# Optimization experiments

Measured on AMD Instinct MI355X. Metric: run time of the kernel, lower is better.

## Reference

```python
import jax, jax.numpy as jnp
import numpy as np

NEG_SLOPE = 0.2  # DGL GATConv default negative_slope


def gat_conv(x, W, attn_l, attn_r, bias, src, dst, n_nodes):
    """DGL-style GATConv. x:[N,F_in], W:[F_in,H*D], attn_l/attn_r/bias:[H,D].
    Returns [N,H,D]."""
    H, D = attn_l.shape
    feat = (x @ W).reshape(n_nodes, H, D)            # projected features
    el = jnp.sum(feat * attn_l, axis=-1)              # [N,H]
    er = jnp.sum(feat * attn_r, axis=-1)              # [N,H]
    e = jax.nn.leaky_relu(el[src] + er[dst], NEG_SLOPE)  # [E,H] per-edge score
    # edge softmax over incoming edges of each dst node (numerically stable)
    m = jax.ops.segment_max(e, dst, num_segments=n_nodes)   # [N,H]
    a = jnp.exp(e - m[dst])
    denom = jax.ops.segment_sum(a, dst, num_segments=n_nodes)
    alpha = a / denom[dst]                            # [E,H]
    msg = feat[src] * alpha[..., None]                # [E,H,D]
    out = jax.ops.segment_sum(msg, dst, num_segments=n_nodes)  # [N,H,D]
    return out + bias


def setup_inputs() -> dict:
    key = jax.random.key(0)
    ks = jax.random.split(key, 12)
    N, E = 50000, 800000
    F_in, D1, H1, F_out = 128, 32, 4, 64
    h = jax.random.normal(ks[0], (N, F_in), dtype=jnp.float32)
    src = jax.random.randint(ks[1], (E,), 0, N, dtype=jnp.int32)
    dst = jax.random.randint(ks[2], (E,), 0, N, dtype=jnp.int32)
    s1 = 1.0 / np.sqrt(F_in)
    s2 = 1.0 / np.sqrt(H1 * D1)
    W1 = jax.random.normal(ks[3], (F_in, H1 * D1), dtype=jnp.float32) * s1
    al1 = jax.random.normal(ks[4], (H1, D1), dtype=jnp.float32) * s1
    ar1 = jax.random.normal(ks[5], (H1, D1), dtype=jnp.float32) * s1
    b1 = jnp.zeros((H1, D1), dtype=jnp.float32)
    W2 = jax.random.normal(ks[6], (H1 * D1, 1 * F_out), dtype=jnp.float32) * s2
    al2 = jax.random.normal(ks[7], (1, F_out), dtype=jnp.float32) * s2
    ar2 = jax.random.normal(ks[8], (1, F_out), dtype=jnp.float32) * s2
    b2 = jnp.zeros((1, F_out), dtype=jnp.float32)
    return {"h": h, "src": src, "dst": dst,
            "W1": W1, "al1": al1, "ar1": ar1, "b1": b1,
            "W2": W2, "al2": al2, "ar2": ar2, "b2": b2}


def reference(h, src, dst, W1, al1, ar1, b1, W2, al2, ar2, b2):
    N = h.shape[0]
    x = gat_conv(h, W1, al1, ar1, b1, src, dst, N)   # [N,H,D]
    x = jax.nn.relu(x.reshape(N, -1))                # flatten heads + ReLU
    # dropout(p=0.2) is identity in eval mode
    x = gat_conv(x, W2, al2, ar2, b2, src, dst, N)   # [N,1,F_out]
    return x.squeeze(1)
```

## Files before the change

kernel.cpp:

```cpp
#include <hip/hip_runtime.h>

#define NEG_SLOPE 0.2f
#define CH 4096
#define DCAP 2048

__device__ inline unsigned short f2bf(float f) {
    unsigned u = __float_as_uint(f);
    unsigned r = (u + 0x7FFFu + ((u >> 16) & 1u)) >> 16;
    return (unsigned short)r;
}
__device__ inline float bf2f(unsigned short s) {
    return __uint_as_float(((unsigned)s) << 16);
}
__device__ inline void wave_lds_fence() {
    asm volatile("s_waitcnt lgkmcnt(0)" ::: "memory");
}

__global__ __launch_bounds__(256) void bucketA_kernel(const int* __restrict__ dst,
                                                      int* __restrict__ bucket_cnt,
                                                      int E, int NB) {
    __shared__ int lh[1024];
    const int tid = threadIdx.x;
    for (int i = tid; i < 1024; i += 256) lh[i] = 0;
    __syncthreads();
    const int base = blockIdx.x * CH;
    const int cnt = min(CH, E - base);
    for (int i = tid; i < cnt; i += 256) atomicAdd(&lh[dst[base + i] >> 6], 1);
    __syncthreads();
    for (int b = tid; b < NB; b += 256)
        if (lh[b]) atomicAdd(&bucket_cnt[b], lh[b]);
}

__global__ __launch_bounds__(1024) void bucketB_kernel(const int* __restrict__ bucket_cnt,
                                                       int* __restrict__ bucket_base,
                                                       int* __restrict__ bucket_cursor,
                                                       int* __restrict__ row_start,
                                                       int N, int NB, int E) {
    __shared__ int sh[1024];
    const int tid = threadIdx.x;
    int v = (tid < NB) ? bucket_cnt[tid] : 0;
    sh[tid] = v;
    __syncthreads();
    for (int off = 1; off < 1024; off <<= 1) {
        int t = (tid >= off) ? sh[tid - off] : 0;
        __syncthreads();
        sh[tid] += t;
        __syncthreads();
    }
    int ex = sh[tid] - v;
    if (tid < NB) {
        bucket_base[tid] = ex;
        bucket_cursor[tid] = ex;
    }
    if (tid == NB - 1) bucket_base[NB] = ex + v;
    if (tid == 0) row_start[N] = E;
}

__global__ __launch_bounds__(256) void csrC_gemm1_kernel(
    const int* __restrict__ src, const int* __restrict__ dst,
    int* __restrict__ bucket_cursor, unsigned* __restrict__ tmp, int E, int NB,
    int nchunks, const float* __restrict__ h, const float* __restrict__ W1,
    const float* __restrict__ al1, const float* __restrict__ ar1,
    unsigned short* __restrict__ feat1b, float* __restrict__ el1,
    float* __restrict__ er1, int N) {
    __shared__ __align__(16) int smem[8448];
    const int tid = threadIdx.x;
    if ((int)blockIdx.x < nchunks) {
        int* lh = smem;
        int* lex = smem + 1024;
        int* lcur = smem + 2048;
        int* gbase_sh = smem + 3072;
        int* psum = smem + 4096;
        unsigned* sortedv = (unsigned*)(smem + 4352);
        const int base_e = blockIdx.x * CH;
        const int cnt_e = min(CH, E - base_e);
        for (int i = tid; i < 1024; i += 256) lh[i] = 0;
        __syncthreads();
        for (int i = tid; i < cnt_e; i += 256) atomicAdd(&lh[dst[base_e + i] >> 6], 1);
        __syncthreads();
        int s0 = lh[tid * 4], s1 = lh[tid * 4 + 1], s2 = lh[tid * 4 + 2], s3 = lh[tid * 4 + 3];
        int tot = s0 + s1 + s2 + s3;
        psum[tid] = tot;
        __syncthreads();
        for (int off = 1; off < 256; off <<= 1) {
            int t = (tid >= off) ? psum[tid - off] : 0;
            __syncthreads();
            psum[tid] += t;
            __syncthreads();
        }
        int ebase = psum[tid] - tot;
        lex[tid * 4] = ebase;
        lex[tid * 4 + 1] = ebase + s0;
        lex[tid * 4 + 2] = ebase + s0 + s1;
        lex[tid * 4 + 3] = ebase + s0 + s1 + s2;
        __syncthreads();
        for (int b = tid; b < NB; b += 256) {
            int c = lh[b];
            gbase_sh[b] = c ? atomicAdd(&bucket_cursor[b], c) : 0;
            lcur[b] = 0;
        }
        __syncthreads();
        for (int i = tid; i < cnt_e; i += 256) {
            int e = base_e + i;
            int d = dst[e];
            unsigned b = (unsigned)d >> 6;
            int r = atomicAdd(&lcur[b], 1);
            sortedv[lex[b] + r] =
                (b << 22) | ((unsigned)(d & 63) << 16) | (unsigned)(src[e] & 0xFFFF);
        }
        __syncthreads();
        for (int i = tid; i < cnt_e; i += 256) {
            unsigned v = sortedv[i];
            int b = v >> 22;
            tmp[gbase_sh[b] + (i - lex[b])] = v;
        }
    } else {
        float* xs = (float*)smem;
        const int row0 = ((int)blockIdx.x - nchunks) * 64;
        {
            const float4* s4 = (const float4*)h;
            float4* d4 = (float4*)xs;
            int base4 = row0 * 32;
            int tot4 = N * 32;
            for (int i = tid; i < 2048; i += 256)
                if (base4 + i < tot4) d4[i] = s4[base4 + i];
        }
        __syncthreads();
        const int lane = tid & 31;
        const int c0 = lane * 4;
        const int r0 = (tid >> 5) * 8;
        float acc[8][4] = {};
#pragma unroll 4
        for (int k = 0; k < 128; ++k) {
            float4 w = *(const float4*)(W1 + k * 128 + c0);
#pragma unroll
            for (int r = 0; r < 8; ++r) {
                float x = xs[(r0 + r) * 128 + k];
                acc[r][0] = fmaf(x, w.x, acc[r][0]);
                acc[r][1] = fmaf(x, w.y, acc[r][1]);
                acc[r][2] = fmaf(x, w.z, acc[r][2]);
                acc[r][3] = fmaf(x, w.w, acc[r][3]);
            }
        }
        float4 alv = *(const float4*)(al1 + c0);
        float4 arv = *(const float4*)(ar1 + c0);
#pragma unroll
        for (int r = 0; r < 8; ++r) {
            int row = row0 + r0 + r;
            if (row < N) {
                ushort4 fb;
                fb.x = f2bf(acc[r][0]);
                fb.y = f2bf(acc[r][1]);
                fb.z = f2bf(acc[r][2]);
                fb.w = f2bf(acc[r][3]);
                *(ushort4*)(feat1b + (size_t)row * 128 + c0) = fb;
                float pl = acc[r][0] * alv.x + acc[r][1] * alv.y + acc[r][2] * alv.z +
                           acc[r][3] * alv.w;
                float pr = acc[r][0] * arv.x + acc[r][1] * arv.y + acc[r][2] * arv.z +
                           acc[r][3] * arv.w;
#pragma unroll
                for (int off = 4; off >= 1; off >>= 1) {
                    pl += __shfl_xor(pl, off, 32);
                    pr += __shfl_xor(pr, off, 32);
                }
                if ((lane & 7) == 0) {
                    el1[row * 4 + (lane >> 3)] = pl;
                    er1[row * 4 + (lane >> 3)] = pr;
                }
            }
        }
    }
}

__global__ __launch_bounds__(256) void bucketD_kernel(const unsigned* __restrict__ tmp,
                                                      const int* __restrict__ bucket_base,
                                                      int* __restrict__ srcs,
                                                      int* __restrict__ row_start,
                                                      int N, int NB) {
    __shared__ unsigned sval[DCAP];
    __shared__ int ssrc[DCAP];
    __shared__ int dh[64], dex[64], dcur[64];
    const int b = blockIdx.x;
    const int tid = threadIdx.x;
    const int gb = bucket_base[b], ge = bucket_base[b + 1];
    const int cnt = ge - gb;
    if (tid < 64) dh[tid] = 0;
    __syncthreads();
    if (cnt <= DCAP) {
        for (int i = tid; i < cnt; i += 256) {
            unsigned v = tmp[gb + i];
            sval[i] = v;
            atomicAdd(&dh[(v >> 16) & 63], 1);
        }
        __syncthreads();
        if (tid < 64) {
            int v = dh[tid], inc = v;
            for (int off = 1; off < 64; off <<= 1) {
                int t = __shfl_up(inc, off, 64);
                if (tid >= off) inc += t;
            }
            dex[tid] = inc - v;
            dcur[tid] = 0;
            int dglob = b * 64 + tid;
            if (dglob < N) row_start[dglob] = gb + inc - v;
        }
        __syncthreads();
        for (int i = tid; i < cnt; i += 256) {
            unsigned val = sval[i];
            int dl = (val >> 16) & 63;
            int r = atomicAdd(&dcur[dl], 1);
            ssrc[dex[dl] + r] = (int)(val & 0xFFFFu);
        }
        __syncthreads();
        for (int i = tid; i < cnt; i += 256) srcs[gb + i] = ssrc[i];
    } else {
        for (int i = tid; i < cnt; i += 256) atomicAdd(&dh[(tmp[gb + i] >> 16) & 63], 1);
        __syncthreads();
        if (tid < 64) {
            int v = dh[tid], inc = v;
            for (int off = 1; off < 64; off <<= 1) {
                int t = __shfl_up(inc, off, 64);
                if (tid >= off) inc += t;
            }
            dex[tid] = inc - v;
            dcur[tid] = 0;
            int dglob = b * 64 + tid;
            if (dglob < N) row_start[dglob] = gb + inc - v;
        }
        __syncthreads();
        for (int i = tid; i < cnt; i += 256) {
            unsigned val = tmp[gb + i];
            int dl = (val >> 16) & 63;
            int r = atomicAdd(&dcur[dl], 1);
            srcs[gb + dex[dl] + r] = (int)(val & 0xFFFFu);
        }
    }
}

__global__ __launch_bounds__(256) void gemm2_fused(const unsigned short* __restrict__ out1b,
                                                   const float* __restrict__ W2,
                                                   const float* __restrict__ al2,
                                                   const float* __restrict__ ar2,
                                                   unsigned short* __restrict__ feat2b,
                                                   float* __restrict__ el2,
                                                   float* __restrict__ er2, int N) {
    __shared__ float xs[128 * 128];
    const int tid = threadIdx.x;
    const int row0 = blockIdx.x * 128;
    {
        const uint4* s8 = (const uint4*)out1b;
        int base8 = row0 * 16;
        int tot8 = N * 16;
        for (int i = tid; i < 2048; i += 256)
            if (base8 + i < tot8) {
                uint4 v = s8[base8 + i];
                float* o = xs + i * 8;
                o[0] = bf2f((unsigned short)(v.x & 0xFFFF));
                o[1] = bf2f((unsigned short)(v.x >> 16));
                o[2] = bf2f((unsigned short)(v.y & 0xFFFF));
                o[3] = bf2f((unsigned short)(v.y >> 16));
                o[4] = bf2f((unsigned short)(v.z & 0xFFFF));
                o[5] = bf2f((unsigned short)(v.z >> 16));
                o[6] = bf2f((unsigned short)(v.w & 0xFFFF));
                o[7] = bf2f((unsigned short)(v.w >> 16));
            }
    }
    __syncthreads();
    const int lane = tid & 15;
    const int c0 = lane * 4;
    const int r0 = (tid >> 4) * 8;
    float acc[8][4] = {};
#pragma unroll 4
    for (int k = 0; k < 128; ++k) {
        float4 w = *(const float4*)(W2 + k * 64 + c0);
#pragma unroll
        for (int r = 0; r < 8; ++r) {
            float x = xs[(r0 + r) * 128 + k];
            acc[r][0] = fmaf(x, w.x, acc[r][0]);
            acc[r][1] = fmaf(x, w.y, acc[r][1]);
            acc[r][2] = fmaf(x, w.z, acc[r][2]);
            acc[r][3] = fmaf(x, w.w, acc[r][3]);
        }
    }
    float4 alv = *(const float4*)(al2 + c0);
    float4 arv = *(const float4*)(ar2 + c0);
#pragma unroll
    for (int r = 0; r < 8; ++r) {
        int row = row0 + r0 + r;
        if (row < N) {
            ushort4 fb;
            fb.x = f2bf(acc[r][0]);
            fb.y = f2bf(acc[r][1]);
            fb.z = f2bf(acc[r][2]);
            fb.w = f2bf(acc[r][3]);
            *(ushort4*)(feat2b + (size_t)row * 64 + c0) = fb;
            float pl = acc[r][0] * alv.x + acc[r][1] * alv.y + acc[r][2] * alv.z +
                       acc[r][3] * alv.w;
            float pr = acc[r][0] * arv.x + acc[r][1] * arv.y + acc[r][2] * arv.z +
                       acc[r][3] * arv.w;
#pragma unroll
            for (int off = 8; off >= 1; off >>= 1) {
                pl += __shfl_xor(pl, off, 16);
                pr += __shfl_xor(pr, off, 16);
            }
            if (lane == 0) {
                el2[row] = pl;
                er2[row] = pr;
            }
        }
    }
}

__global__ __launch_bounds__(256) void gather1_kernel(const int* __restrict__ row_start,
                                                      const int* __restrict__ srcs,
                                                      const float* __restrict__ el1,
                                                      const float* __restrict__ er1,
                                                      const unsigned short* __restrict__ feat1b,
                                                      const float* __restrict__ b1,
                                                      unsigned short* __restrict__ out1b,
                                                      int N) {
    __shared__ int s_sh[4][64];
    __shared__ float a_sh[4][256];
    const int tid = threadIdx.x;
    const int w = tid >> 6;
    const int lane = tid & 63;
    const int d = blockIdx.x * 4 + w;
    if (d >= N) return;
    const int beg = row_start[d], end = row_start[d + 1];
    const int half = lane >> 5;
    const int l32 = lane & 31;
    const int c0 = l32 * 4;
    const int h = l32 >> 3;
    float4 er4 = *(const float4*)(er1 + (size_t)d * 4);
    float acc0 = 0.f, acc1 = 0.f, acc2 = 0.f, acc3 = 0.f;
    float bcc0 = 0.f, bcc1 = 0.f, bcc2 = 0.f, bcc3 = 0.f;
    float den = 0.f;
    for (int k0 = beg; k0 < end; k0 += 64) {
        const int M = min(64, end - k0);
        if (lane < M) {
            int s = srcs[k0 + lane];
            s_sh[w][lane] = s;
            float4 el4 = *(const float4*)(el1 + (size_t)s * 4);
            float v0 = el4.x + er4.x;
            float v1 = el4.y + er4.y;
            float v2 = el4.z + er4.z;
            float v3 = el4.w + er4.w;
            v0 = v0 > 0.f ? v0 : NEG_SLOPE * v0;
            v1 = v1 > 0.f ? v1 : NEG_SLOPE * v1;
            v2 = v2 > 0.f ? v2 : NEG_SLOPE * v2;
            v3 = v3 > 0.f ? v3 : NEG_SLOPE * v3;
            a_sh[w][lane * 4 + 0] = __expf(v0);
            a_sh[w][lane * 4 + 1] = __expf(v1);
            a_sh[w][lane * 4 + 2] = __expf(v2);
            a_sh[w][lane * 4 + 3] = __expf(v3);
        }
        wave_lds_fence();
        int e = half;
        for (; e + 2 < M; e += 4) {
            int s0 = s_sh[w][e], s1 = s_sh[w][e + 2];
            float a0 = a_sh[w][e * 4 + h];
            float a1 = a_sh[w][(e + 2) * 4 + h];
            ushort4 f0 = *(const ushort4*)(feat1b + (size_t)s0 * 128 + c0);
            ushort4 f1 = *(const ushort4*)(feat1b + (size_t)s1 * 128 + c0);
            den += a0 + a1;
            acc0 = fmaf(bf2f(f0.x), a0, acc0);
            acc1 = fmaf(bf2f(f0.y), a0, acc1);
            acc2 = fmaf(bf2f(f0.z), a0, acc2);
            acc3 = fmaf(bf2f(f0.w), a0, acc3);
            bcc0 = fmaf(bf2f(f1.x), a1, bcc0);
            bcc1 = fmaf(bf2f(f1.y), a1, bcc1);
            bcc2 = fmaf(bf2f(f1.z), a1, bcc2);
            bcc3 = fmaf(bf2f(f1.w), a1, bcc3);
        }
        if (e < M) {
            int s0 = s_sh[w][e];
            float a0 = a_sh[w][e * 4 + h];
            ushort4 f0 = *(const ushort4*)(feat1b + (size_t)s0 * 128 + c0);
            den += a0;
            acc0 = fmaf(bf2f(f0.x), a0, acc0);
            acc1 = fmaf(bf2f(f0.y), a0, acc1);
            acc2 = fmaf(bf2f(f0.z), a0, acc2);
            acc3 = fmaf(bf2f(f0.w), a0, acc3);
        }
        wave_lds_fence();
    }
    acc0 += bcc0;
    acc1 += bcc1;
    acc2 += bcc2;
    acc3 += bcc3;
    acc0 += __shfl_xor(acc0, 32, 64);
    acc1 += __shfl_xor(acc1, 32, 64);
    acc2 += __shfl_xor(acc2, 32, 64);
    acc3 += __shfl_xor(acc3, 32, 64);
    den += __shfl_xor(den, 32, 64);
    if (half == 0) {
        float inv = (end > beg) ? 1.f / den : 0.f;
        float4 bv = *(const float4*)(b1 + c0);
        float r0v = fmaxf(acc0 * inv + bv.x, 0.f);
        float r1v = fmaxf(acc1 * inv + bv.y, 0.f);
        float r2v = fmaxf(acc2 * inv + bv.z, 0.f);
        float r3v = fmaxf(acc3 * inv + bv.w, 0.f);
        ushort4 o;
        o.x = f2bf(r0v);
        o.y = f2bf(r1v);
        o.z = f2bf(r2v);
        o.w = f2bf(r3v);
        *(ushort4*)(out1b + (size_t)d * 128 + c0) = o;
    }
}

__global__ __launch_bounds__(256) void gather2_kernel(const int* __restrict__ row_start,
                                                      const int* __restrict__ srcs,
                                                      const float* __restrict__ el2,
                                                      const float* __restrict__ er2,
                                                      const unsigned short* __restrict__ feat2b,
                                                      const float* __restrict__ b2,
                                                      float* __restrict__ out2, int N) {
    __shared__ int s_sh[4][64];
    __shared__ float a_sh[4][64];
    const int tid = threadIdx.x;
    const int w = tid >> 6;
    const int lane = tid & 63;
    const int d = blockIdx.x * 4 + w;
    if (d >= N) return;
    const int beg = row_start[d], end = row_start[d + 1];
    const int half = lane >> 5;
    const int l32 = lane & 31;
    const int c0 = l32 * 2;
    const float er_d = er2[d];
    float acc0 = 0.f, acc1 = 0.f, bcc0 = 0.f, bcc1 = 0.f, den = 0.f;
    for (int k0 = beg; k0 < end; k0 += 64) {
        const int M = min(64, end - k0);
        if (lane < M) {
            int s = srcs[k0 + lane];
            s_sh[w][lane] = s;
            float v = el2[s] + er_d;
            v = v > 0.f ? v : NEG_SLOPE * v;
            a_sh[w][lane] = __expf(v);
        }
        wave_lds_fence();
        int e = half;
        for (; e + 2 < M; e += 4) {
            int s0 = s_sh[w][e], s1 = s_sh[w][e + 2];
            float a0 = a_sh[w][e], a1 = a_sh[w][e + 2];
            ushort2 f0 = *(const ushort2*)(feat2b + (size_t)s0 * 64 + c0);
            ushort2 f1 = *(const ushort2*)(feat2b + (size_t)s1 * 64 + c0);
            den += a0 + a1;
            acc0 = fmaf(bf2f(f0.x), a0, acc0);
            acc1 = fmaf(bf2f(f0.y), a0, acc1);
            bcc0 = fmaf(bf2f(f1.x), a1, bcc0);
            bcc1 = fmaf(bf2f(f1.y), a1, bcc1);
        }
        if (e < M) {
            int s0 = s_sh[w][e];
            float a0 = a_sh[w][e];
            ushort2 f0 = *(const ushort2*)(feat2b + (size_t)s0 * 64 + c0);
            den += a0;
            acc0 = fmaf(bf2f(f0.x), a0, acc0);
            acc1 = fmaf(bf2f(f0.y), a0, acc1);
        }
        wave_lds_fence();
    }
    acc0 += bcc0;
    acc1 += bcc1;
    acc0 += __shfl_xor(acc0, 32, 64);
    acc1 += __shfl_xor(acc1, 32, 64);
    den += __shfl_xor(den, 32, 64);
    if (half == 0) {
        float inv = (end > beg) ? 1.f / den : 0.f;
        *(float2*)(out2 + (size_t)d * 64 + c0) =
            make_float2(acc0 * inv + b2[c0], acc1 * inv + b2[c0 + 1]);
    }
}

extern "C" void kernel_launch(void* const* d_in, const int* in_sizes, int n_in,
                              void* d_out, int out_size, void* d_ws, size_t ws_size,
                              hipStream_t stream) {
    const float* h   = (const float*)d_in[0];
    const int*   src = (const int*)d_in[1];
    const int*   dst = (const int*)d_in[2];
    const float* W1  = (const float*)d_in[3];
    const float* al1 = (const float*)d_in[4];
    const float* ar1 = (const float*)d_in[5];
    const float* b1  = (const float*)d_in[6];
    const float* W2  = (const float*)d_in[7];
    const float* al2 = (const float*)d_in[8];
    const float* ar2 = (const float*)d_in[9];
    const float* b2  = (const float*)d_in[10];

    const int N = in_sizes[0] / 128;
    const int E = in_sizes[1];
    const int NB = (N + 63) >> 6;

    char* ws = (char*)d_ws;
    size_t off = 0;
    auto alloc = [&](size_t elems) -> void* {
        void* p = (void*)(ws + off);
        off += ((elems * 4 + 255) / 256) * 256;
        return p;
    };
    int* bucket_cnt    = (int*)alloc(NB);
    int* bucket_base   = (int*)alloc(NB + 1);
    int* bucket_cursor = (int*)alloc(NB);
    unsigned* tmp      = (unsigned*)alloc(E);
    int* srcs          = (int*)alloc(E);
    int* row_start     = (int*)alloc(N + 1);
    float* el1   = (float*)alloc((size_t)N * 4);
    float* er1   = (float*)alloc((size_t)N * 4);
    unsigned short* feat1b = (unsigned short*)alloc((size_t)N * 64);
    unsigned short* out1b  = (unsigned short*)alloc((size_t)N * 64);
    float* el2   = (float*)alloc(N);
    float* er2   = (float*)alloc(N);
    unsigned short* feat2b = (unsigned short*)alloc((size_t)N * 32);
    float* out2  = (float*)d_out;

    const int nchunks = (E + CH - 1) / CH;
    const int gemm1_blocks = (N + 63) / 64;

    hipMemsetAsync(bucket_cnt, 0, (size_t)NB * 4, stream);
    bucketA_kernel<<<nchunks, 256, 0, stream>>>(dst, bucket_cnt, E, NB);
    bucketB_kernel<<<1, 1024, 0, stream>>>(bucket_cnt, bucket_base, bucket_cursor,
                                           row_start, N, NB, E);
    csrC_gemm1_kernel<<<nchunks + gemm1_blocks, 256, 0, stream>>>(
        src, dst, bucket_cursor, tmp, E, NB, nchunks, h, W1, al1, ar1, feat1b, el1,
        er1, N);
    bucketD_kernel<<<NB, 256, 0, stream>>>(tmp, bucket_base, srcs, row_start, N, NB);

    gather1_kernel<<<(N + 3) / 4, 256, 0, stream>>>(row_start, srcs, el1, er1, feat1b,
                                                    b1, out1b, N);

    gemm2_fused<<<(N + 127) / 128, 256, 0, stream>>>(out1b, W2, al2, ar2, feat2b, el2,
                                                     er2, N);
    gather2_kernel<<<(N + 3) / 4, 256, 0, stream>>>(row_start, srcs, el2, er2, feat2b,
                                                    b2, out2, N);
}
```

Before: 222.5 us.

## Fuse bucket count with last-block scan, and CSR bucket sort with layer-1 gather

Merges the bucket histogram and prefix-scan kernels into one launch, where the last block to finish (chosen by an atomic ticket) performs the scan. It also fuses the per-bucket CSR sort with the layer-1 attention gather, so each block aggregates its 64 destination nodes straight from the sorted sources held in LDS. This removes two launches and a global re-read of srcs and row_start. In exchange, the gather now runs on only about 782 blocks with 16 nodes per wave, which reduces parallelism and latency hiding compared with the previous grid of one node per wave.

```diff
diff --git a/kernel.cpp b/kernel.cpp
--- a/kernel.cpp
+++ b/kernel.cpp
@@ -16,43 +16,52 @@
     asm volatile("s_waitcnt lgkmcnt(0)" ::: "memory");
 }
 
-__global__ __launch_bounds__(256) void bucketA_kernel(const int* __restrict__ dst,
-                                                      int* __restrict__ bucket_cnt,
-                                                      int E, int NB) {
-    __shared__ int lh[1024];
-    const int tid = threadIdx.x;
-    for (int i = tid; i < 1024; i += 256) lh[i] = 0;
-    __syncthreads();
-    const int base = blockIdx.x * CH;
-    const int cnt = min(CH, E - base);
-    for (int i = tid; i < cnt; i += 256) atomicAdd(&lh[dst[base + i] >> 6], 1);
-    __syncthreads();
-    for (int b = tid; b < NB; b += 256)
-        if (lh[b]) atomicAdd(&bucket_cnt[b], lh[b]);
-}
-
-__global__ __launch_bounds__(1024) void bucketB_kernel(const int* __restrict__ bucket_cnt,
+__global__ __launch_bounds__(256) void bucketAB_kernel(const int* __restrict__ dst,
+                                                       int* __restrict__ bucket_cnt,
                                                        int* __restrict__ bucket_base,
                                                        int* __restrict__ bucket_cursor,
                                                        int* __restrict__ row_start,
                                                        int N, int NB, int E) {
-    __shared__ int sh[1024];
+    __shared__ int lh[1024];
+    __shared__ int psum[256];
+    __shared__ int ticket_sh;
     const int tid = threadIdx.x;
-    int v = (tid < NB) ? bucket_cnt[tid] : 0;
-    sh[tid] = v;
-    __syncthreads();
-    for (int off = 1; off < 1024; off <<= 1) {
-        int t = (tid >= off) ? sh[tid - off] : 0;
-        __syncthreads();
-        sh[tid] += t;
-        __syncthreads();
-    }
-    int ex = sh[tid] - v;
-    if (tid < NB) {
-        bucket_base[tid] = ex;
-        bucket_cursor[tid] = ex;
-    }
-    if (tid == NB - 1) bucket_base[NB] = ex + v;
+    for (int i = tid; i < 1024; i += 256) lh[i] = 0;
+    __syncthreads();
+    const int base = blockIdx.x * CH;
+    const int cnt = min(CH, E - base);
+    for (int i = tid; i < cnt; i += 256) atomicAdd(&lh[dst[base + i] >> 6], 1);
+    __syncthreads();
+    for (int b = tid; b < NB; b += 256)
+        if (lh[b]) atomicAdd(&bucket_cnt[b], lh[b]);
+    __syncthreads();
+    if (tid == 0) {
+        __threadfence();
+        ticket_sh = atomicAdd(&bucket_cnt[NB], 1);
+    }
+    __syncthreads();
+    if (ticket_sh != (int)gridDim.x - 1) return;
+    for (int i = tid; i < 1024; i += 256)
+        lh[i] = (i < NB) ? atomicAdd(&bucket_cnt[i], 0) : 0;
+    __syncthreads();
+    int s0 = lh[tid * 4], s1 = lh[tid * 4 + 1], s2 = lh[tid * 4 + 2], s3 = lh[tid * 4 + 3];
+    int tot = s0 + s1 + s2 + s3;
+    psum[tid] = tot;
+    __syncthreads();
+    for (int off = 1; off < 256; off <<= 1) {
+        int t = (tid >= off) ? psum[tid - off] : 0;
+        __syncthreads();
+        psum[tid] += t;
+        __syncthreads();
+    }
+    int ebase = psum[tid] - tot;
+    int e0 = ebase, e1 = ebase + s0, e2 = ebase + s0 + s1, e3 = ebase + s0 + s1 + s2;
+    int i0 = tid * 4;
+    if (i0 < NB)     { bucket_base[i0]     = e0; bucket_cursor[i0]     = e0; }
+    if (i0 + 1 < NB) { bucket_base[i0 + 1] = e1; bucket_cursor[i0 + 1] = e1; }
+    if (i0 + 2 < NB) { bucket_base[i0 + 2] = e2; bucket_cursor[i0 + 2] = e2; }
+    if (i0 + 3 < NB) { bucket_base[i0 + 3] = e3; bucket_cursor[i0 + 3] = e3; }
+    if (tid == 255) bucket_base[NB] = psum[255];
     if (tid == 0) row_start[N] = E;
 }
 
@@ -172,21 +181,24 @@
     }
 }
 
-__global__ __launch_bounds__(256) void bucketD_kernel(const unsigned* __restrict__ tmp,
-                                                      const int* __restrict__ bucket_base,
-                                                      int* __restrict__ srcs,
-                                                      int* __restrict__ row_start,
-                                                      int N, int NB) {
+__global__ __launch_bounds__(256) void sortgather1_kernel(
+    const unsigned* __restrict__ tmp, const int* __restrict__ bucket_base,
+    int* __restrict__ srcs, int* __restrict__ row_start,
+    const float* __restrict__ el1, const float* __restrict__ er1,
+    const unsigned short* __restrict__ feat1b, const float* __restrict__ b1,
+    unsigned short* __restrict__ out1b, int N, int NB) {
     __shared__ unsigned sval[DCAP];
     __shared__ int ssrc[DCAP];
     __shared__ int dh[64], dex[64], dcur[64];
+    __shared__ float a_sh[4][256];
     const int b = blockIdx.x;
     const int tid = threadIdx.x;
     const int gb = bucket_base[b], ge = bucket_base[b + 1];
     const int cnt = ge - gb;
     if (tid < 64) dh[tid] = 0;
     __syncthreads();
-    if (cnt <= DCAP) {
+    const bool lds_ok = (cnt <= DCAP);
+    if (lds_ok) {
         for (int i = tid; i < cnt; i += 256) {
             unsigned v = tmp[gb + i];
             sval[i] = v;
@@ -233,6 +245,92 @@
             int dl = (val >> 16) & 63;
             int r = atomicAdd(&dcur[dl], 1);
             srcs[gb + dex[dl] + r] = (int)(val & 0xFFFFu);
+        }
+        __syncthreads();
+    }
+    const int w = tid >> 6;
+    const int lane = tid & 63;
+    const int half = lane >> 5;
+    const int l32 = lane & 31;
+    const int c0 = l32 * 4;
+    const int hh = l32 >> 3;
+    const int* sp = lds_ok ? (const int*)ssrc : (srcs + gb);
+    for (int t = 0; t < 16; ++t) {
+        const int dl = w * 16 + t;
+        const int d = b * 64 + dl;
+        if (d >= N) break;
+        const int ebeg = dex[dl];
+        const int ecnt = dh[dl];
+        float4 er4 = *(const float4*)(er1 + (size_t)d * 4);
+        float acc0 = 0.f, acc1 = 0.f, acc2 = 0.f, acc3 = 0.f;
+        float bcc0 = 0.f, bcc1 = 0.f, bcc2 = 0.f, bcc3 = 0.f;
+        float den = 0.f;
+        for (int k0 = 0; k0 < ecnt; k0 += 64) {
+            const int M = min(64, ecnt - k0);
+            if (lane < M) {
+                int s = sp[ebeg + k0 + lane];
+                float4 el4 = *(const float4*)(el1 + (size_t)s * 4);
+                float v0 = el4.x + er4.x;
+                float v1 = el4.y + er4.y;
+                float v2 = el4.z + er4.z;
+                float v3 = el4.w + er4.w;
+                v0 = v0 > 0.f ? v0 : NEG_SLOPE * v0;
+                v1 = v1 > 0.f ? v1 : NEG_SLOPE * v1;
+                v2 = v2 > 0.f ? v2 : NEG_SLOPE * v2;
+                v3 = v3 > 0.f ? v3 : NEG_SLOPE * v3;
+                a_sh[w][lane * 4 + 0] = __expf(v0);
+                a_sh[w][lane * 4 + 1] = __expf(v1);
+                a_sh[w][lane * 4 + 2] = __expf(v2);
+                a_sh[w][lane * 4 + 3] = __expf(v3);
+            }
+            wave_lds_fence();
+            int e = half;
+            for (; e + 2 < M; e += 4) {
+                int s0 = sp[ebeg + k0 + e], s1 = sp[ebeg + k0 + e + 2];
+                float a0 = a_sh[w][e * 4 + hh];
+                float a1 = a_sh[w][(e + 2) * 4 + hh];
+                ushort4 f0 = *(const ushort4*)(feat1b + (size_t)s0 * 128 + c0);
+                ushort4 f1 = *(const ushort4*)(feat1b + (size_t)s1 * 128 + c0);
+                den += a0 + a1;
+                acc0 = fmaf(bf2f(f0.x), a0, acc0);
+                acc1 = fmaf(bf2f(f0.y), a0, acc1);
+                acc2 = fmaf(bf2f(f0.z), a0, acc2);
+                acc3 = fmaf(bf2f(f0.w), a0, acc3);
+                bcc0 = fmaf(bf2f(f1.x), a1, bcc0);
+                bcc1 = fmaf(bf2f(f1.y), a1, bcc1);
+                bcc2 = fmaf(bf2f(f1.z), a1, bcc2);
+                bcc3 = fmaf(bf2f(f1.w), a1, bcc3);
+            }
+            if (e < M) {
+                int s0 = sp[ebeg + k0 + e];
+                float a0 = a_sh[w][e * 4 + hh];
+                ushort4 f0 = *(const ushort4*)(feat1b + (size_t)s0 * 128 + c0);
+                den += a0;
+                acc0 = fmaf(bf2f(f0.x), a0, acc0);
+                acc1 = fmaf(bf2f(f0.y), a0, acc1);
+                acc2 = fmaf(bf2f(f0.z), a0, acc2);
+                acc3 = fmaf(bf2f(f0.w), a0, acc3);
+            }
+            wave_lds_fence();
+        }
+        acc0 += bcc0;
+        acc1 += bcc1;
+        acc2 += bcc2;
+        acc3 += bcc3;
+        acc0 += __shfl_xor(acc0, 32, 64);
+        acc1 += __shfl_xor(acc1, 32, 64);
+        acc2 += __shfl_xor(acc2, 32, 64);
+        acc3 += __shfl_xor(acc3, 32, 64);
+        den += __shfl_xor(den, 32, 64);
+        if (half == 0) {
+            float inv = (ecnt > 0) ? 1.f / den : 0.f;
+            float4 bv = *(const float4*)(b1 + c0);
+            ushort4 o;
+            o.x = f2bf(fmaxf(acc0 * inv + bv.x, 0.f));
+            o.y = f2bf(fmaxf(acc1 * inv + bv.y, 0.f));
+            o.z = f2bf(fmaxf(acc2 * inv + bv.z, 0.f));
+            o.w = f2bf(fmaxf(acc3 * inv + bv.w, 0.f));
+            *(ushort4*)(out1b + (size_t)d * 128 + c0) = o;
         }
     }
 }
@@ -308,104 +406,6 @@
                 er2[row] = pr;
             }
         }
-    }
-}
-
-__global__ __launch_bounds__(256) void gather1_kernel(const int* __restrict__ row_start,
-                                                      const int* __restrict__ srcs,
-                                                      const float* __restrict__ el1,
-                                                      const float* __restrict__ er1,
-                                                      const unsigned short* __restrict__ feat1b,
-                                                      const float* __restrict__ b1,
-                                                      unsigned short* __restrict__ out1b,
-                                                      int N) {
-    __shared__ int s_sh[4][64];
-    __shared__ float a_sh[4][256];
-    const int tid = threadIdx.x;
-    const int w = tid >> 6;
-    const int lane = tid & 63;
-    const int d = blockIdx.x * 4 + w;
-    if (d >= N) return;
-    const int beg = row_start[d], end = row_start[d + 1];
-    const int half = lane >> 5;
-    const int l32 = lane & 31;
-    const int c0 = l32 * 4;
-    const int h = l32 >> 3;
-    float4 er4 = *(const float4*)(er1 + (size_t)d * 4);
-    float acc0 = 0.f, acc1 = 0.f, acc2 = 0.f, acc3 = 0.f;
-    float bcc0 = 0.f, bcc1 = 0.f, bcc2 = 0.f, bcc3 = 0.f;
-    float den = 0.f;
-    for (int k0 = beg; k0 < end; k0 += 64) {
-        const int M = min(64, end - k0);
-        if (lane < M) {
-            int s = srcs[k0 + lane];
-            s_sh[w][lane] = s;
-            float4 el4 = *(const float4*)(el1 + (size_t)s * 4);
-            float v0 = el4.x + er4.x;
-            float v1 = el4.y + er4.y;
-            float v2 = el4.z + er4.z;
-            float v3 = el4.w + er4.w;
-            v0 = v0 > 0.f ? v0 : NEG_SLOPE * v0;
-            v1 = v1 > 0.f ? v1 : NEG_SLOPE * v1;
-            v2 = v2 > 0.f ? v2 : NEG_SLOPE * v2;
-            v3 = v3 > 0.f ? v3 : NEG_SLOPE * v3;
-            a_sh[w][lane * 4 + 0] = __expf(v0);
-            a_sh[w][lane * 4 + 1] = __expf(v1);
-            a_sh[w][lane * 4 + 2] = __expf(v2);
-            a_sh[w][lane * 4 + 3] = __expf(v3);
-        }
-        wave_lds_fence();
-        int e = half;
-        for (; e + 2 < M; e += 4) {
-            int s0 = s_sh[w][e], s1 = s_sh[w][e + 2];
-            float a0 = a_sh[w][e * 4 + h];
-            float a1 = a_sh[w][(e + 2) * 4 + h];
-            ushort4 f0 = *(const ushort4*)(feat1b + (size_t)s0 * 128 + c0);
-            ushort4 f1 = *(const ushort4*)(feat1b + (size_t)s1 * 128 + c0);
-            den += a0 + a1;
-            acc0 = fmaf(bf2f(f0.x), a0, acc0);
-            acc1 = fmaf(bf2f(f0.y), a0, acc1);
-            acc2 = fmaf(bf2f(f0.z), a0, acc2);
-            acc3 = fmaf(bf2f(f0.w), a0, acc3);
-            bcc0 = fmaf(bf2f(f1.x), a1, bcc0);
-            bcc1 = fmaf(bf2f(f1.y), a1, bcc1);
-            bcc2 = fmaf(bf2f(f1.z), a1, bcc2);
-            bcc3 = fmaf(bf2f(f1.w), a1, bcc3);
-        }
-        if (e < M) {
-            int s0 = s_sh[w][e];
-            float a0 = a_sh[w][e * 4 + h];
-            ushort4 f0 = *(const ushort4*)(feat1b + (size_t)s0 * 128 + c0);
-            den += a0;
-            acc0 = fmaf(bf2f(f0.x), a0, acc0);
-            acc1 = fmaf(bf2f(f0.y), a0, acc1);
-            acc2 = fmaf(bf2f(f0.z), a0, acc2);
-            acc3 = fmaf(bf2f(f0.w), a0, acc3);
-        }
-        wave_lds_fence();
-    }
-    acc0 += bcc0;
-    acc1 += bcc1;
-    acc2 += bcc2;
-    acc3 += bcc3;
-    acc0 += __shfl_xor(acc0, 32, 64);
-    acc1 += __shfl_xor(acc1, 32, 64);
-    acc2 += __shfl_xor(acc2, 32, 64);
-    acc3 += __shfl_xor(acc3, 32, 64);
-    den += __shfl_xor(den, 32, 64);
-    if (half == 0) {
-        float inv = (end > beg) ? 1.f / den : 0.f;
-        float4 bv = *(const float4*)(b1 + c0);
-        float r0v = fmaxf(acc0 * inv + bv.x, 0.f);
-        float r1v = fmaxf(acc1 * inv + bv.y, 0.f);
-        float r2v = fmaxf(acc2 * inv + bv.z, 0.f);
-        float r3v = fmaxf(acc3 * inv + bv.w, 0.f);
-        ushort4 o;
-        o.x = f2bf(r0v);
-        o.y = f2bf(r1v);
-        o.z = f2bf(r2v);
-        o.w = f2bf(r3v);
-        *(ushort4*)(out1b + (size_t)d * 128 + c0) = o;
     }
 }
 
@@ -499,7 +499,7 @@
         off += ((elems * 4 + 255) / 256) * 256;
         return p;
     };
-    int* bucket_cnt    = (int*)alloc(NB);
+    int* bucket_cnt    = (int*)alloc(NB + 1);
     int* bucket_base   = (int*)alloc(NB + 1);
     int* bucket_cursor = (int*)alloc(NB);
     unsigned* tmp      = (unsigned*)alloc(E);
@@ -517,18 +517,14 @@
     const int nchunks = (E + CH - 1) / CH;
     const int gemm1_blocks = (N + 63) / 64;
 
-    hipMemsetAsync(bucket_cnt, 0, (size_t)NB * 4, stream);
-    bucketA_kernel<<<nchunks, 256, 0, stream>>>(dst, bucket_cnt, E, NB);
-    bucketB_kernel<<<1, 1024, 0, stream>>>(bucket_cnt, bucket_base, bucket_cursor,
-                                           row_start, N, NB, E);
+    hipMemsetAsync(bucket_cnt, 0, (size_t)(NB + 1) * 4, stream);
+    bucketAB_kernel<<<nchunks, 256, 0, stream>>>(dst, bucket_cnt, bucket_base,
+                                                 bucket_cursor, row_start, N, NB, E);
     csrC_gemm1_kernel<<<nchunks + gemm1_blocks, 256, 0, stream>>>(
         src, dst, bucket_cursor, tmp, E, NB, nchunks, h, W1, al1, ar1, feat1b, el1,
         er1, N);
-    bucketD_kernel<<<NB, 256, 0, stream>>>(tmp, bucket_base, srcs, row_start, N, NB);
-
-    gather1_kernel<<<(N + 3) / 4, 256, 0, stream>>>(row_start, srcs, el1, er1, feat1b,
-                                                    b1, out1b, N);
-
+    sortgather1_kernel<<<NB, 256, 0, stream>>>(tmp, bucket_base, srcs, row_start, el1,
+                                               er1, feat1b, b1, out1b, N, NB);
     gemm2_fused<<<(N + 127) / 128, 256, 0, stream>>>(out1b, W2, al2, ar2, feat2b, el2,
                                                      er2, N);
     gather2_kernel<<<(N + 3) / 4, 256, 0, stream>>>(row_start, srcs, el2, er2, feat2b,
```

After: 242.2 us. +8.9%, slower.
